# Kernel optimization log

Hardware: AMD Instinct MI355X
Metric: run time of the kernel (lower is better)

The kernel has to match this reference:

```python
import jax, jax.numpy as jnp
import numpy as np


def setup_inputs() -> dict:
    key = jax.random.key(0)
    k1, k2 = jax.random.split(key)
    B, S, H, D = 4, 2048, 12, 64
    v = jax.random.normal(k1, (B, S, H, D), dtype=jnp.float32)
    # learned per-head positional weights, sorted ascending along last dim
    # (mirrors torch.sort(torch.randn(H, S), dim=-1)[0])
    w = jnp.sort(jax.random.normal(k2, (H, S), dtype=jnp.float32), axis=-1)
    return {"v": v, "w": w}


def reference(v, w):
    # PositionalBias._naive
    # v: [B, S, H, D]; w: [H, S_max]
    B, S, H, D = v.shape
    seq_len = S - 2  # v[:, 1:-1] is the non-special-token span
    w_ = w[:, :seq_len]  # [H, seq_len]
    # _construct_bias builds bias[h, l, j] = w[h, |l - j|] (symmetric Toeplitz)
    pos = jnp.arange(seq_len)
    idx = jnp.abs(pos[:, None] - pos[None, :])  # [seq_len, seq_len]
    bias = w_[:, idx]  # [H, seq_len, seq_len]
    # zero-pad one row/col on each side -> [H, S, S]
    bias = jnp.pad(bias, ((0, 0), (1, 1), (1, 1)))
    # z_pb: [1, S, H]
    z_pb = jnp.sum(bias, axis=-1).T[None, :, :]
    # pbv: [B, S, H, D]
    pbv = jnp.einsum('nlhd,hlj->njhd', v, bias)
    return (pbv, z_pb)
```

## Files before the change

### kernel.cpp

```cpp
#include <hip/hip_runtime.h>
#include <hip/hip_bf16.h>


typedef short short8 __attribute__((ext_vector_type(8)));
typedef float floatx4 __attribute__((ext_vector_type(4)));

#define TL 2280

__device__ __forceinline__ unsigned short f2bf(float f) {
  union { __hip_bfloat16 b; unsigned short u; } cv;
  cv.b = __float2bfloat16(f);
  return cv.u;
}

__global__ __launch_bounds__(256, 3) void fused_kernel(const float* __restrict__ v,
                                                       const float* __restrict__ w,
                                                       float* __restrict__ out) {
  __shared__ __attribute__((aligned(16))) short Tls[8 * TL];

  const int bx  = blockIdx.x;
  const int tid = threadIdx.x;

  if (bx >= 768) {
    const int h = bx - 768;
    float* wv  = (float*)Tls;
    float* pfx = ((float*)Tls) + 2048;
    __shared__ float wsum[4];
    const float* wh = w + (size_t)h * 2048;
    float* zout = out + 6291456;
    for (int i = tid; i < 2048; i += 256) wv[i] = (i < 2046) ? wh[i] : 0.f;
    __syncthreads();
    const int base = tid * 8;
    float run0 = 0.f;
    #pragma unroll
    for (int k = 0; k < 8; ++k) run0 += wv[base + k];
    float x = run0;
    #pragma unroll
    for (int dd = 1; dd < 64; dd <<= 1) {
      float y = __shfl_up(x, dd);
      if ((tid & 63) >= dd) x += y;
    }
    if ((tid & 63) == 63) wsum[tid >> 6] = x;
    __syncthreads();
    const int wid4 = tid >> 6;
    float woff = 0.f;
    #pragma unroll
    for (int u = 0; u < 3; ++u) { float t = wsum[u]; if (u < wid4) woff += t; }
    float pr = x + woff - run0;
    #pragma unroll
    for (int k = 0; k < 8; ++k) { pr += wv[base + k]; pfx[base + k] = pr; }
    __syncthreads();
    for (int i = tid; i < 2046; i += 256) {
      float z = pfx[i] + pfx[2045 - i] - wv[0];
      zout[(size_t)(i + 1) * 12 + h] = z;
    }
    if (tid == 0) { zout[h] = 0.f; zout[(size_t)2047 * 12 + h] = 0.f; }
    return;
  }

  const int slice = bx % 48;
  const int jt    = bx / 48;
  const int ndt = slice & 3;
  const int h   = slice >> 2;
  const int lane = tid & 63, wid = tid >> 6;
  const int lm = lane & 15, quad = lane >> 4;
  const int jb = jt * 128;
  const int strip = ndt * 64 + wid * 16;
  const int d = (strip + lm) & 63;

  const float* vrow = v + (((size_t)ndt * 2048) * 12 + h) * 64 + d;

  float r0[16], rA[16];
  {
    const int lb = quad * 8;
    #pragma unroll
    for (int i = 0; i < 8; ++i) r0[i]     = vrow[(size_t)(lb + i) * 768];
    #pragma unroll
    for (int i = 0; i < 8; ++i) r0[8 + i] = vrow[(size_t)(lb + 32 + i) * 768];
    #pragma unroll
    for (int i = 0; i < 8; ++i) rA[i]     = vrow[(size_t)(64 + lb + i) * 768];
    #pragma unroll
    for (int i = 0; i < 8; ++i) rA[8 + i] = vrow[(size_t)(64 + lb + 32 + i) * 768];
  }

  const float* wh = w + (size_t)h * 2048;
  for (int g = tid; g < 8 * (TL / 8); g += 256) {
    int c  = g / (TL / 8);
    int p8 = (g - c * (TL / 8)) * 8;
    unsigned short buf[8] __attribute__((aligned(16)));
    #pragma unroll
    for (int i = 0; i < 8; ++i) {
      int t = 127 + jb - (p8 + i) - c;
      int a = t < 0 ? -t : t;
      buf[i] = (a <= 2045) ? f2bf(wh[a]) : (unsigned short)0;
    }
    *(short8*)&Tls[c * TL + p8] = *(const short8*)buf;
  }
  __syncthreads();

  auto packB = [&](int t, const float* f, short8& b0, short8& b1) {
    const int lb = t * 64 + quad * 8;
    #pragma unroll
    for (int i = 0; i < 8; ++i) {
      int la = lb + i, lc = lb + 32 + i;
      b0[i] = (la == 0 || la == 2047) ? (short)0 : (short)f2bf(f[i]);
      b1[i] = (lc == 0 || lc == 2047) ? (short)0 : (short)f2bf(f[8 + i]);
    }
  };

  const int pbase = 127 + quad * 8 - lm;
  auto load_af = [&](int p0) -> short8 {
    int c = p0 & 7;
    return *(const short8*)&Tls[c * TL + (p0 - c)];
  };

  short8 afr[10];
  #pragma unroll
  for (int i = 0; i < 10; ++i) afr[i] = load_af((i - 7) * 16 + pbase);

  short8 bc0, bc1;
  packB(0, r0, bc0, bc1);

  floatx4 acc[8];
  #pragma unroll
  for (int ma = 0; ma < 8; ++ma) acc[ma] = (floatx4){0.f, 0.f, 0.f, 0.f};

  #pragma unroll 4
  for (int t = 0; t < 32; ++t) {
    const int l0 = t * 64;
    float rN[16];
    const int lb2 = ((t < 30) ? t + 2 : 31) * 64 + quad * 8;
    #pragma unroll
    for (int i = 0; i < 8; ++i) rN[i]     = vrow[(size_t)(lb2 + i) * 768];
    #pragma unroll
    for (int i = 0; i < 8; ++i) rN[8 + i] = vrow[(size_t)(lb2 + 32 + i) * 768];
    const int l0n = (t < 31) ? l0 + 64 : l0;
    short8 na0 = load_af(l0n - 16 + pbase);
    short8 na1 = load_af(l0n      + pbase);
    short8 na2 = load_af(l0n + 16 + pbase);
    short8 na3 = load_af(l0n + 32 + pbase);

    #pragma unroll
    for (int ma = 0; ma < 8; ++ma)
      acc[ma] = __builtin_amdgcn_mfma_f32_16x16x32_bf16(afr[7 - ma], bc0, acc[ma], 0, 0, 0);
    #pragma unroll
    for (int ma = 0; ma < 8; ++ma)
      acc[ma] = __builtin_amdgcn_mfma_f32_16x16x32_bf16(afr[9 - ma], bc1, acc[ma], 0, 0, 0);

    packB((t < 31) ? t + 1 : 31, rA, bc0, bc1);

    #pragma unroll
    for (int i = 0; i < 6; ++i) afr[i] = afr[i + 4];
    afr[6] = na0; afr[7] = na1; afr[8] = na2; afr[9] = na3;
    #pragma unroll
    for (int i = 0; i < 16; ++i) rA[i] = rN[i];
  }

  float* obase = out + (size_t)ndt * 1572864 + (size_t)h * 64 + d;
  #pragma unroll
  for (int ma = 0; ma < 8; ++ma) {
    floatx4 cc = acc[ma];
    #pragma unroll
    for (int r = 0; r < 4; ++r) {
      int j = jb + ma * 16 + quad * 4 + r;
      float val = (j == 0 || j == 2047) ? 0.f : cc[r];
      obase[(size_t)j * 768] = val;
    }
  }
}

extern "C" void kernel_launch(void* const* d_in, const int* in_sizes, int n_in,
                              void* d_out, int out_size, void* d_ws, size_t ws_size,
                              hipStream_t stream) {
  const float* v = (const float*)d_in[0];
  const float* w = (const float*)d_in[1];
  float* out = (float*)d_out;
  fused_kernel<<<dim3(780), 256, 0, stream>>>(v, w, out);
}
```

Baseline: 119.5 us.

## Pre-transpose v to bf16 in a separate prep kernel before GEMM

Splits the fused kernel in two. A prep kernel converts v to bf16 once and transposes it into a global buffer laid out so that l is contiguous per (n,h,d), zeroing the padded rows; it also computes z_pb. The GEMM kernel then reads B fragments as 16-byte vector loads instead of strided fp32 scalar loads with per-iteration conversion. This trades an extra kernel launch plus a write and re-read of a bf16 copy of v for cheaper, coalesced loads and less register pressure in the main loop.

New measurement: 129.7 us. +8.6%, slower.

```diff
diff --git a/kernel.cpp b/kernel.cpp
--- a/kernel.cpp
+++ b/kernel.cpp
@@ -7,33 +7,35 @@
 
 #define TL 2280
 
+__device__ __attribute__((aligned(16))) short g_vt[4 * 12 * 64 * 2048];
+
 __device__ __forceinline__ unsigned short f2bf(float f) {
   union { __hip_bfloat16 b; unsigned short u; } cv;
   cv.b = __float2bfloat16(f);
   return cv.u;
 }
 
-__global__ __launch_bounds__(256, 3) void fused_kernel(const float* __restrict__ v,
-                                                       const float* __restrict__ w,
-                                                       float* __restrict__ out) {
-  __shared__ __attribute__((aligned(16))) short Tls[8 * TL];
+__global__ __launch_bounds__(256) void prep_kernel(const float* __restrict__ v,
+                                                   const float* __restrict__ w,
+                                                   float* __restrict__ out) {
+  __shared__ float zls[4096];
+  __shared__ float wsum[4];
 
   const int bx  = blockIdx.x;
   const int tid = threadIdx.x;
 
-  if (bx >= 768) {
-    const int h = bx - 768;
-    float* wv  = (float*)Tls;
-    float* pfx = ((float*)Tls) + 2048;
-    __shared__ float wsum[4];
+  if (bx >= 384) {
+    const int h = bx - 384;
+    float* wvv = zls;
+    float* pfx = zls + 2048;
     const float* wh = w + (size_t)h * 2048;
     float* zout = out + 6291456;
-    for (int i = tid; i < 2048; i += 256) wv[i] = (i < 2046) ? wh[i] : 0.f;
+    for (int i = tid; i < 2048; i += 256) wvv[i] = (i < 2046) ? wh[i] : 0.f;
     __syncthreads();
     const int base = tid * 8;
     float run0 = 0.f;
     #pragma unroll
-    for (int k = 0; k < 8; ++k) run0 += wv[base + k];
+    for (int k = 0; k < 8; ++k) run0 += wvv[base + k];
     float x = run0;
     #pragma unroll
     for (int dd = 1; dd < 64; dd <<= 1) {
@@ -48,15 +50,47 @@
     for (int u = 0; u < 3; ++u) { float t = wsum[u]; if (u < wid4) woff += t; }
     float pr = x + woff - run0;
     #pragma unroll
-    for (int k = 0; k < 8; ++k) { pr += wv[base + k]; pfx[base + k] = pr; }
+    for (int k = 0; k < 8; ++k) { pr += wvv[base + k]; pfx[base + k] = pr; }
     __syncthreads();
     for (int i = tid; i < 2046; i += 256) {
-      float z = pfx[i] + pfx[2045 - i] - wv[0];
+      float z = pfx[i] + pfx[2045 - i] - wvv[0];
       zout[(size_t)(i + 1) * 12 + h] = z;
     }
     if (tid == 0) { zout[h] = 0.f; zout[(size_t)2047 * 12 + h] = 0.f; }
     return;
   }
+
+  const int chunk = bx & 7;
+  const int slice = bx >> 3;
+  const int n = slice / 12, h = slice - n * 12;
+  const int lane = tid & 63;
+  const int wv   = tid >> 6;
+  const int l0 = chunk * 256 + wv * 64;
+
+  const float* src = v + (((size_t)n * 2048 + l0) * 12 + h) * 64 + lane;
+  short* dst = g_vt + (((size_t)n * 12 + h) * 64 + lane) * 2048 + l0;
+
+  #pragma unroll
+  for (int k = 0; k < 8; ++k) {
+    float f[8];
+    #pragma unroll
+    for (int i = 0; i < 8; ++i) f[i] = src[(size_t)(k * 8 + i) * 768];
+    short8 b;
+    #pragma unroll
+    for (int i = 0; i < 8; ++i) {
+      int l = l0 + k * 8 + i;
+      b[i] = (l == 0 || l == 2047) ? (short)0 : (short)f2bf(f[i]);
+    }
+    *(short8*)&dst[k * 8] = b;
+  }
+}
+
+__global__ __launch_bounds__(256, 3) void gemm_kernel(const float* __restrict__ w,
+                                                      float* __restrict__ out) {
+  __shared__ __attribute__((aligned(16))) short Tls[8 * TL];
+
+  const int bx  = blockIdx.x;
+  const int tid = threadIdx.x;
 
   const int slice = bx % 48;
   const int jt    = bx / 48;
@@ -65,23 +99,12 @@
   const int lane = tid & 63, wid = tid >> 6;
   const int lm = lane & 15, quad = lane >> 4;
   const int jb = jt * 128;
-  const int strip = ndt * 64 + wid * 16;
-  const int d = (strip + lm) & 63;
+  const int d  = wid * 16 + lm;
 
-  const float* vrow = v + (((size_t)ndt * 2048) * 12 + h) * 64 + d;
+  const short* vtb = g_vt + (((size_t)ndt * 12 + h) * 64 + d) * 2048;
 
-  float r0[16], rA[16];
-  {
-    const int lb = quad * 8;
-    #pragma unroll
-    for (int i = 0; i < 8; ++i) r0[i]     = vrow[(size_t)(lb + i) * 768];
-    #pragma unroll
-    for (int i = 0; i < 8; ++i) r0[8 + i] = vrow[(size_t)(lb + 32 + i) * 768];
-    #pragma unroll
-    for (int i = 0; i < 8; ++i) rA[i]     = vrow[(size_t)(64 + lb + i) * 768];
-    #pragma unroll
-    for (int i = 0; i < 8; ++i) rA[8 + i] = vrow[(size_t)(64 + lb + 32 + i) * 768];
-  }
+  short8 bc0 = *(const short8*)&vtb[quad * 8];
+  short8 bc1 = *(const short8*)&vtb[32 + quad * 8];
 
   const float* wh = w + (size_t)h * 2048;
   for (int g = tid; g < 8 * (TL / 8); g += 256) {
@@ -98,16 +121,6 @@
   }
   __syncthreads();
 
-  auto packB = [&](int t, const float* f, short8& b0, short8& b1) {
-    const int lb = t * 64 + quad * 8;
-    #pragma unroll
-    for (int i = 0; i < 8; ++i) {
-      int la = lb + i, lc = lb + 32 + i;
-      b0[i] = (la == 0 || la == 2047) ? (short)0 : (short)f2bf(f[i]);
-      b1[i] = (lc == 0 || lc == 2047) ? (short)0 : (short)f2bf(f[8 + i]);
-    }
-  };
-
   const int pbase = 127 + quad * 8 - lm;
   auto load_af = [&](int p0) -> short8 {
     int c = p0 & 7;
@@ -118,9 +131,6 @@
   #pragma unroll
   for (int i = 0; i < 10; ++i) afr[i] = load_af((i - 7) * 16 + pbase);
 
-  short8 bc0, bc1;
-  packB(0, r0, bc0, bc1);
-
   floatx4 acc[8];
   #pragma unroll
   for (int ma = 0; ma < 8; ++ma) acc[ma] = (floatx4){0.f, 0.f, 0.f, 0.f};
@@ -128,12 +138,9 @@
   #pragma unroll 4
   for (int t = 0; t < 32; ++t) {
     const int l0 = t * 64;
-    float rN[16];
-    const int lb2 = ((t < 30) ? t + 2 : 31) * 64 + quad * 8;
-    #pragma unroll
-    for (int i = 0; i < 8; ++i) rN[i]     = vrow[(size_t)(lb2 + i) * 768];
-    #pragma unroll
-    for (int i = 0; i < 8; ++i) rN[8 + i] = vrow[(size_t)(lb2 + 32 + i) * 768];
+    const int lb = ((t < 31) ? (t + 1) : 31) * 64 + quad * 8;
+    short8 bn0 = *(const short8*)&vtb[lb];
+    short8 bn1 = *(const short8*)&vtb[lb + 32];
     const int l0n = (t < 31) ? l0 + 64 : l0;
     short8 na0 = load_af(l0n - 16 + pbase);
     short8 na1 = load_af(l0n      + pbase);
@@ -147,13 +154,10 @@
     for (int ma = 0; ma < 8; ++ma)
       acc[ma] = __builtin_amdgcn_mfma_f32_16x16x32_bf16(afr[9 - ma], bc1, acc[ma], 0, 0, 0);
 
-    packB((t < 31) ? t + 1 : 31, rA, bc0, bc1);
-
+    bc0 = bn0; bc1 = bn1;
     #pragma unroll
     for (int i = 0; i < 6; ++i) afr[i] = afr[i + 4];
     afr[6] = na0; afr[7] = na1; afr[8] = na2; afr[9] = na3;
-    #pragma unroll
-    for (int i = 0; i < 16; ++i) rA[i] = rN[i];
   }
 
   float* obase = out + (size_t)ndt * 1572864 + (size_t)h * 64 + d;
@@ -175,5 +179,6 @@
   const float* v = (const float*)d_in[0];
   const float* w = (const float*)d_in[1];
   float* out = (float*)d_out;
-  fused_kernel<<<dim3(780), 256, 0, stream>>>(v, w, out);
+  prep_kernel<<<dim3(396), 256, 0, stream>>>(v, w, out);
+  gemm_kernel<<<dim3(768), 256, 0, stream>>>(w, out);
 }
```
